# Optimization experiments

Hardware: AMD Instinct MI355X
Metric: run time of the kernel (lower is better)

The kernel has to match this reference:

```python
import jax, jax.numpy as jnp
import numpy as np

N = 16384      # number of nodes (pos rows)
S = 16384      # number of src nodes (src_pos rows)
E = 262144     # number of edges (COO entries)
D = 512        # embed_dim
H = 8          # num_heads
HD = D // H    # head_dim = 64
HID = 1024     # mlp hidden
MLP_IN = D + 3 * H  # 536
EPS = 1e-5


def layer_norm(x, g, b):
    mu = jnp.mean(x, axis=-1, keepdims=True)
    var = jnp.mean((x - mu) ** 2, axis=-1, keepdims=True)
    return (x - mu) * jax.lax.rsqrt(var + EPS) * g + b


def setup_inputs() -> dict:
    key = jax.random.key(0)
    ks = jax.random.split(key, 20)
    s = 1.0 / np.sqrt(D)
    sh = 1.0 / np.sqrt(HID)
    return {
        "x": jax.random.normal(ks[0], (N, D), jnp.float32),
        "Wq": jax.random.uniform(ks[1], (D, D), jnp.float32, -s, s),
        "bq": jnp.zeros((D,), jnp.float32),
        "Wk": jax.random.uniform(ks[2], (D, D), jnp.float32, -s, s),
        "bk": jnp.zeros((D,), jnp.float32),
        "g_att": jnp.ones((D,), jnp.float32),
        "b_att": jnp.zeros((D,), jnp.float32),
        "g_mlp": jnp.ones((D,), jnp.float32),
        "b_mlp": jnp.zeros((D,), jnp.float32),
        "W_in": jax.random.uniform(ks[3], (HID, MLP_IN), jnp.float32, -s, s),
        "b_in": jnp.zeros((HID,), jnp.float32),
        "W_out": jax.random.uniform(ks[4], (D, HID), jnp.float32, -sh, sh),
        "b_out": jnp.zeros((D,), jnp.float32),
        "att_bias": jax.random.normal(ks[5], (H, E), jnp.float32),
        "dist": jax.random.uniform(ks[6], (E,), jnp.float32, 0.5, 6.0),
        "pos": jax.random.normal(ks[7], (N, 3), jnp.float32),
        "src_pos": jax.random.normal(ks[8], (S, 3), jnp.float32),
        "row_index": jax.random.randint(ks[9], (E,), 0, N),
        "src_index": jax.random.randint(ks[10], (E,), 0, S),
        "org_to_src": jax.random.randint(ks[11], (S,), 0, N),
    }


def reference(x, Wq, bq, Wk, bk, g_att, b_att, g_mlp, b_mlp, W_in, b_in,
              W_out, b_out, att_bias, dist, pos, src_pos,
              row_index, src_index, org_to_src):
    n = x.shape[0]
    z = layer_norm(x, g_att, b_att)
    q = (z @ Wq.T + bq).reshape(n, H, HD)          # [N,H,hd]
    k = (z @ Wk.T + bk).reshape(n, H, HD)          # [N,H,hd]
    k_src = k[org_to_src]                          # [S,H,hd]
    # per-edge masked logits: q[row] . k_src[col] / sqrt(hd) + bias
    qe = q[row_index]                              # [E,H,hd]
    ke = k_src[src_index]                          # [E,H,hd]
    logits = jnp.einsum('ehd,ehd->eh', qe, ke) / jnp.sqrt(jnp.float32(HD))
    logits = logits + att_bias.T                   # [E,H]
    # segment (per-row) softmax over incident edges
    m = jax.ops.segment_max(logits, row_index, num_segments=n)
    p = jnp.exp(logits - m[row_index])
    den = jax.ops.segment_sum(p, row_index, num_segments=n)
    att = p / den[row_index]                       # [E,H]
    inv = jnp.where(dist == 0, 0.0, 1.0 / dist)[:, None]
    att = att * inv
    # sparse bmm: feat[h,row] += att * src_pos[col]; rowsum for centering
    sp = src_pos[src_index]                        # [E,3]
    feat = jax.ops.segment_sum(att[:, :, None] * sp[:, None, :],
                               row_index, num_segments=n)   # [N,H,3]
    rowsum = jax.ops.segment_sum(att, row_index, num_segments=n)  # [N,H]
    feat = feat - rowsum[:, :, None] * pos[:, None, :]
    feat = feat.reshape(n, H * 3)
    z2 = layer_norm(x, g_mlp, b_mlp)
    h = jax.nn.gelu(jnp.concatenate([z2, feat], axis=-1) @ W_in.T + b_in)
    return x + (h @ W_out.T + b_out)
```

## Files before the change

### kernel.cpp

```cpp
#include <hip/hip_runtime.h>
#include <math.h>


typedef unsigned short u16;
typedef __attribute__((ext_vector_type(8))) short bf16x8;
typedef __attribute__((ext_vector_type(4))) float f32x4;
typedef __attribute__((ext_vector_type(2))) float f32x2;

constexpr int N_NODES = 16384;
constexpr int E_EDGES = 262144;
constexpr int D = 512;
constexpr int KIN = 576;

constexpr size_t OFF_ZATT = 0;
constexpr size_t OFF_ZCAT = 16777216;
constexpr size_t OFF_WQK  = 35651584;
constexpr size_t OFF_BQK  = 36700160;
constexpr size_t OFF_WIN  = 36704256;
constexpr size_t OFF_WOUT = 37883904;
constexpr size_t OFF_QK   = 38932480;
constexpr size_t OFF_CNT  = 55709696;
constexpr size_t OFF_BKT  = 55775232;
constexpr size_t OFF_HBF  = 59969536;

static __device__ __forceinline__ u16 f2bf(float f) {
  union { float f; unsigned int u; } v; v.f = f;
  unsigned int u = v.u;
  u = u + 0x7FFFu + ((u >> 16) & 1u);
  return (u16)(u >> 16);
}
static __device__ __forceinline__ void gload16(const u16* g, u16* l) {
  __builtin_amdgcn_global_load_lds(
      (const __attribute__((address_space(1))) unsigned int*)g,
      (__attribute__((address_space(3))) unsigned int*)l, 16, 0, 0);
}

__global__ __launch_bounds__(256) void prep_weights(
    const float* __restrict__ Wq, const float* __restrict__ Wk,
    const float* __restrict__ bq, const float* __restrict__ bk,
    const float* __restrict__ W_in, const float* __restrict__ W_out,
    const int* __restrict__ row_index,
    const float* __restrict__ att_bias, const float* __restrict__ dist,
    const float* __restrict__ src_pos, const int* __restrict__ src_index,
    const int* __restrict__ org_to_src,
    u16* __restrict__ wqk, float* __restrict__ bqk,
    u16* __restrict__ win, u16* __restrict__ wout,
    int* __restrict__ cnt, int* __restrict__ bucket, float* __restrict__ rec)
{
  const int gid = blockIdx.x * 256 + threadIdx.x;
  if (gid < 512 * 1024) {
    wqk[gid]  = f2bf(gid < 512 * 512 ? Wq[gid] : Wk[gid - 512 * 512]);
    wout[gid] = f2bf(W_out[gid]);
  }
  if (gid < 1024 * KIN) {
    const int r = gid / KIN, c = gid - r * KIN;
    win[gid] = f2bf(c < 536 ? W_in[r * 536 + c] : 0.f);
  }
  if (gid < 1024) bqk[gid] = gid < 512 ? bq[gid] : bk[gid - 512];
  if (gid < E_EDGES) {
    const int r = row_index[gid];
    const int p = atomicAdd(&cnt[r], 1);
    if (p < 64) bucket[(size_t)r * 64 + p] = gid;
    const int s = src_index[gid];
    const float dv = dist[gid];
    float4 q0, q1, q2, q3;
    q0.x = att_bias[gid];
    q0.y = att_bias[(size_t)1 * E_EDGES + gid];
    q0.z = att_bias[(size_t)2 * E_EDGES + gid];
    q0.w = att_bias[(size_t)3 * E_EDGES + gid];
    q1.x = att_bias[(size_t)4 * E_EDGES + gid];
    q1.y = att_bias[(size_t)5 * E_EDGES + gid];
    q1.z = att_bias[(size_t)6 * E_EDGES + gid];
    q1.w = att_bias[(size_t)7 * E_EDGES + gid];
    q2.x = (dv == 0.f) ? 0.f : 1.f / dv;
    q2.y = src_pos[(size_t)s * 3 + 0];
    q2.z = src_pos[(size_t)s * 3 + 1];
    q2.w = src_pos[(size_t)s * 3 + 2];
    q3.x = __int_as_float(org_to_src[s]);
    q3.y = 0.f; q3.z = 0.f; q3.w = 0.f;
    float4* rg = (float4*)(rec + (size_t)gid * 16);
    rg[0] = q0; rg[1] = q1; rg[2] = q2; rg[3] = q3;
  }
}

__global__ __launch_bounds__(256) void ln_kernel(
    const float* __restrict__ x,
    const float* __restrict__ g1, const float* __restrict__ b1,
    const float* __restrict__ g2, const float* __restrict__ b2,
    u16* __restrict__ zatt, u16* __restrict__ zcat)
{
  const int row = blockIdx.x;
  const int t = threadIdx.x;
  const float2 v = *(const float2*)(x + (size_t)row * D + t * 2);
  float s = v.x + v.y;
  float s2 = v.x * v.x + v.y * v.y;
#pragma unroll
  for (int m = 1; m < 64; m <<= 1) {
    s  += __shfl_xor(s, m, 64);
    s2 += __shfl_xor(s2, m, 64);
  }
  __shared__ float red[8];
  const int wv = t >> 6;
  if ((t & 63) == 0) { red[wv] = s; red[4 + wv] = s2; }
  __syncthreads();
  s  = red[0] + red[1] + red[2] + red[3];
  s2 = red[4] + red[5] + red[6] + red[7];
  const float mu = s * (1.f / D);
  const float var = s2 * (1.f / D) - mu * mu;
  const float rs = rsqrtf(var + 1e-5f);
  const int c0 = t * 2;
  const float n0 = (v.x - mu) * rs, n1 = (v.y - mu) * rs;
  zatt[(size_t)row * D + c0]       = f2bf(n0 * g1[c0] + b1[c0]);
  zatt[(size_t)row * D + c0 + 1]   = f2bf(n1 * g1[c0 + 1] + b1[c0 + 1]);
  zcat[(size_t)row * KIN + c0]     = f2bf(n0 * g2[c0] + b2[c0]);
  zcat[(size_t)row * KIN + c0 + 1] = f2bf(n1 * g2[c0 + 1] + b2[c0 + 1]);
  if (t < 64) zcat[(size_t)row * KIN + D + t] = 0;
}

template <int EPI, int WPE>
__global__ __launch_bounds__(256, WPE) void gemm_nt(
    const u16* __restrict__ A, const u16* __restrict__ B,
    const float* __restrict__ bias, const float* __restrict__ resid,
    void* __restrict__ Cout, int M, int Nn, int K)
{
  constexpr int BM = 128, BN = 128, BK = 32;
  __shared__ __align__(16) u16 As[2 * BM * BK];
  __shared__ __align__(16) u16 Bs[2 * BN * BK];
  const int tid = threadIdx.x;
  const int lane = tid & 63;
  const int wave = tid >> 6;
  const int m0 = blockIdx.x * BM;
  const int n0 = blockIdx.y * BN;
  const int wm = (wave >> 1) * 64;
  const int wn = (wave & 1) * 64;
  const int fr = lane & 15;
  const int fq = lane >> 4;
  const int srow = lane >> 2;
  const int skoff = (lane & 3) * 8;

  f32x4 acc[4][4];
#pragma unroll
  for (int i = 0; i < 4; ++i)
#pragma unroll
    for (int j = 0; j < 4; ++j) acc[i][j] = 0.f;

  for (int k0 = 0; k0 < K; k0 += 2 * BK) {
    __syncthreads();
#pragma unroll
    for (int t = 0; t < 2; ++t) {
#pragma unroll
      for (int r = 0; r < 2; ++r) {
        const int rowbase = r * 64 + wave * 16;
        gload16(A + (size_t)(m0 + rowbase + srow) * K + k0 + t * BK + skoff,
                As + t * (BM * BK) + rowbase * BK);
        gload16(B + (size_t)(n0 + rowbase + srow) * K + k0 + t * BK + skoff,
                Bs + t * (BN * BK) + rowbase * BK);
      }
    }
    __syncthreads();
#pragma unroll
    for (int t = 0; t < 2; ++t) {
      bf16x8 af[4], bfr[4];
#pragma unroll
      for (int mi = 0; mi < 4; ++mi)
        af[mi] = *(const bf16x8*)(As + t * (BM * BK) + (wm + mi * 16 + fr) * BK + fq * 8);
#pragma unroll
      for (int ni = 0; ni < 4; ++ni)
        bfr[ni] = *(const bf16x8*)(Bs + t * (BN * BK) + (wn + ni * 16 + fr) * BK + fq * 8);
#pragma unroll
      for (int mi = 0; mi < 4; ++mi)
#pragma unroll
        for (int ni = 0; ni < 4; ++ni)
          acc[mi][ni] = __builtin_amdgcn_mfma_f32_16x16x32_bf16(af[mi], bfr[ni], acc[mi][ni], 0, 0, 0);
    }
  }

#pragma unroll
  for (int mi = 0; mi < 4; ++mi) {
#pragma unroll
    for (int ni = 0; ni < 4; ++ni) {
      const int col = n0 + wn + ni * 16 + fr;
      const float bv = bias[col];
#pragma unroll
      for (int rr = 0; rr < 4; ++rr) {
        const int row = m0 + wm + mi * 16 + fq * 4 + rr;
        float v = acc[mi][ni][rr] + bv;
        if (EPI == 1) {
          const float nu = -1.5957691216057308f * (v + 0.044715f * v * v * v);
          const float sg = __builtin_amdgcn_rcpf(1.f + __expf(nu));
          ((u16*)Cout)[(size_t)row * Nn + col] = f2bf(v * sg);
        } else if (EPI == 2) {
          ((float*)Cout)[(size_t)row * Nn + col] = v + resid[(size_t)row * Nn + col];
        } else {
          const int pk = __builtin_amdgcn_cvt_pk_fp8_f32(v, v, 0, false);
          ((unsigned char*)Cout)[(size_t)row * Nn + col] = (unsigned char)(pk & 0xFF);
        }
      }
    }
  }
}

__global__ __launch_bounds__(256) void edge_csr(
    const unsigned char* __restrict__ qk8, const float* __restrict__ rec,
    const int* __restrict__ cnt, const int* __restrict__ bucket,
    const float* __restrict__ pos, u16* __restrict__ zcat)
{
  const int lane = threadIdx.x & 63;
  const int wave = threadIdx.x >> 6;
  const int row = blockIdx.x * 4 + wave;
  const int half = lane >> 5;
  const int sub = lane & 31;
  const int h = sub >> 2, j = sub & 3;
  const int deg = min(cnt[row], 64);
  const int base = row * 64;

  const uint4 qv = *(const uint4*)(qk8 + (size_t)row * 1024 + sub * 16);
  float qf[16];
  {
    const unsigned int* qu = (const unsigned int*)&qv;
#pragma unroll
    for (int i = 0; i < 4; ++i) {
      const f32x2 lo = __builtin_amdgcn_cvt_pk_f32_fp8(qu[i], false);
      const f32x2 hi = __builtin_amdgcn_cvt_pk_f32_fp8(qu[i], true);
      qf[i * 4 + 0] = lo.x; qf[i * 4 + 1] = lo.y;
      qf[i * 4 + 2] = hi.x; qf[i * 4 + 3] = hi.y;
    }
  }

  float accA = 0.f, accB = 0.f;
  const int npair = (deg + 1) >> 1;

  bool ok0 = half < deg;
  int e0 = ok0 ? bucket[base + half] : 0;
  const float* r0 = rec + (size_t)e0 * 16;
  float bias0 = r0[h];
  float invd0 = r0[8];
  float spA0 = (j >= 2) ? r0[7 + j] : 0.f;
  float spB0 = (j == 1) ? r0[11] : 0.f;
  uint4 kv0 = *(const uint4*)(qk8 + (size_t)__float_as_int(r0[12]) * 1024 + 512 + sub * 16);

  bool ok1 = 2 + half < deg;
  int e1 = ok1 ? bucket[base + 2 + half] : 0;
  const float* r1 = rec + (size_t)e1 * 16;
  float bias1 = r1[h];
  float invd1 = r1[8];
  float spA1 = (j >= 2) ? r1[7 + j] : 0.f;
  float spB1 = (j == 1) ? r1[11] : 0.f;
  int kr1 = __float_as_int(r1[12]);

  bool ok2 = 4 + half < deg;
  int e2 = ok2 ? bucket[base + 4 + half] : 0;

  for (int i = 0; i < npair; ++i) {
    const uint4 kv1 = *(const uint4*)(qk8 + (size_t)kr1 * 1024 + 512 + sub * 16);
    const float* r2 = rec + (size_t)e2 * 16;
    const float bias2 = r2[h];
    const float invd2 = r2[8];
    const float spA2 = (j >= 2) ? r2[7 + j] : 0.f;
    const float spB2 = (j == 1) ? r2[11] : 0.f;
    const int kr2 = __float_as_int(r2[12]);
    const bool ok3 = 2 * (i + 3) + half < deg;
    const int e3 = ok3 ? bucket[base + 2 * (i + 3) + half] : 0;

    float p;
    {
      const unsigned int* ku = (const unsigned int*)&kv0;
      const f32x2 a0 = __builtin_amdgcn_cvt_pk_f32_fp8(ku[0], false);
      const f32x2 a1 = __builtin_amdgcn_cvt_pk_f32_fp8(ku[0], true);
      const f32x2 b0 = __builtin_amdgcn_cvt_pk_f32_fp8(ku[1], false);
      const f32x2 b1 = __builtin_amdgcn_cvt_pk_f32_fp8(ku[1], true);
      const f32x2 c0 = __builtin_amdgcn_cvt_pk_f32_fp8(ku[2], false);
      const f32x2 c1 = __builtin_amdgcn_cvt_pk_f32_fp8(ku[2], true);
      const f32x2 d0 = __builtin_amdgcn_cvt_pk_f32_fp8(ku[3], false);
      const f32x2 d1 = __builtin_amdgcn_cvt_pk_f32_fp8(ku[3], true);
      p = qf[0] * a0.x;
      p = fmaf(qf[1],  a0.y, p);  p = fmaf(qf[2],  a1.x, p);  p = fmaf(qf[3],  a1.y, p);
      p = fmaf(qf[4],  b0.x, p);  p = fmaf(qf[5],  b0.y, p);  p = fmaf(qf[6],  b1.x, p);
      p = fmaf(qf[7],  b1.y, p);  p = fmaf(qf[8],  c0.x, p);  p = fmaf(qf[9],  c0.y, p);
      p = fmaf(qf[10], c1.x, p);  p = fmaf(qf[11], c1.y, p);  p = fmaf(qf[12], d0.x, p);
      p = fmaf(qf[13], d0.y, p);  p = fmaf(qf[14], d1.x, p);  p = fmaf(qf[15], d1.y, p);
    }
    p += __shfl_xor(p, 1, 64);
    p += __shfl_xor(p, 2, 64);
    float pe = __expf(p * 0.125f + bias0);
    pe = ok0 ? pe : 0.f;
    const float w = pe * invd0;
    accA += (j == 0) ? pe : (j == 1) ? w : w * spA0;
    accB += w * spB0;

    ok0 = ok1; bias0 = bias1; invd0 = invd1; spA0 = spA1; spB0 = spB1; kv0 = kv1;
    ok1 = ok2; bias1 = bias2; invd1 = invd2; spA1 = spA2; spB1 = spB2; kr1 = kr2;
    ok2 = ok3; e2 = e3;
  }

  accA += __shfl_xor(accA, 32, 64);
  accB += __shfl_xor(accB, 32, 64);
  const int hb = h << 2;
  const float den  = __shfl(accA, hb + 0, 64);
  const float wsum = __shfl(accA, hb + 1, 64);
  const float wsp01 = __shfl(accA, hb + 2 + (j & 1), 64);
  const float wsp2  = __shfl(accB, hb + 1, 64);
  const float invd = (den != 0.f) ? 1.f / den : 0.f;
  const float rsum = wsum * invd;
  if (half == 0 && j < 3) {
    const float wspj = (j < 2) ? wsp01 : wsp2;
    zcat[(size_t)row * KIN + D + h * 3 + j] = f2bf(wspj * invd - rsum * pos[row * 3 + j]);
  }
}

extern "C" void kernel_launch(void* const* d_in, const int* in_sizes, int n_in,
                              void* d_out, int out_size, void* d_ws, size_t ws_size,
                              hipStream_t stream)
{
  const float* x        = (const float*)d_in[0];
  const float* Wq       = (const float*)d_in[1];
  const float* bq       = (const float*)d_in[2];
  const float* Wk       = (const float*)d_in[3];
  const float* bk       = (const float*)d_in[4];
  const float* g_att    = (const float*)d_in[5];
  const float* b_att    = (const float*)d_in[6];
  const float* g_mlp    = (const float*)d_in[7];
  const float* b_mlp    = (const float*)d_in[8];
  const float* W_in     = (const float*)d_in[9];
  const float* b_in     = (const float*)d_in[10];
  const float* W_out    = (const float*)d_in[11];
  const float* b_out    = (const float*)d_in[12];
  const float* att_bias = (const float*)d_in[13];
  const float* dist     = (const float*)d_in[14];
  const float* pos      = (const float*)d_in[15];
  const float* src_pos  = (const float*)d_in[16];
  const int* row_index  = (const int*)d_in[17];
  const int* src_index  = (const int*)d_in[18];
  const int* org_to_src = (const int*)d_in[19];

  char* ws = (char*)d_ws;
  u16*   zatt = (u16*)(ws + OFF_ZATT);
  u16*   zcat = (u16*)(ws + OFF_ZCAT);
  u16*   wqk  = (u16*)(ws + OFF_WQK);
  float* bqk  = (float*)(ws + OFF_BQK);
  u16*   win  = (u16*)(ws + OFF_WIN);
  u16*   wout = (u16*)(ws + OFF_WOUT);
  unsigned char* qk8 = (unsigned char*)(ws + OFF_QK);
  int*   cnt  = (int*)(ws + OFF_CNT);
  int*   bkt  = (int*)(ws + OFF_BKT);
  u16*   hbf  = (u16*)(ws + OFF_HBF);
  float* rec  = (float*)(ws + OFF_HBF);

  hipMemsetAsync(ws + OFF_CNT, 0, 65536, stream);

  prep_weights<<<2304, 256, 0, stream>>>(Wq, Wk, bq, bk, W_in, W_out, row_index,
                                         att_bias, dist, src_pos, src_index, org_to_src,
                                         wqk, bqk, win, wout, cnt, bkt, rec);
  ln_kernel<<<N_NODES, 256, 0, stream>>>(x, g_att, b_att, g_mlp, b_mlp, zatt, zcat);
  gemm_nt<4, 4><<<dim3(128, 8), 256, 0, stream>>>(zatt, wqk, bqk, nullptr, qk8, N_NODES, 1024, 512);
  edge_csr<<<N_NODES / 4, 256, 0, stream>>>(qk8, rec, cnt, bkt, pos, zcat);
  gemm_nt<1, 4><<<dim3(128, 8), 256, 0, stream>>>(zcat, win, b_in, nullptr, hbf, N_NODES, 1024, KIN);
  gemm_nt<2, 2><<<dim3(128, 4), 256, 0, stream>>>(hbf, wout, b_out, x, d_out, N_NODES, 512, 1024);
}
```

Before: 268.0 us.

## Add 256x256-tile 8-wave pipelined GEMM for QK and MLP-in projections

```diff
diff --git a/kernel.cpp b/kernel.cpp
--- a/kernel.cpp
+++ b/kernel.cpp
@@ -117,6 +117,144 @@
   if (t < 64) zcat[(size_t)row * KIN + D + t] = 0;
 }
 
+
+#define MM_BLK(AF, BF, NB) do {                                               \
+  __builtin_amdgcn_s_setprio(1);                                              \
+  _Pragma("unroll")                                                           \
+  for (int mi = 0; mi < 8; ++mi) {                                            \
+    acc[mi][NB]     = __builtin_amdgcn_mfma_f32_16x16x32_bf16(AF[mi], BF[0], acc[mi][NB], 0, 0, 0);     \
+    acc[mi][NB + 1] = __builtin_amdgcn_mfma_f32_16x16x32_bf16(AF[mi], BF[1], acc[mi][NB + 1], 0, 0, 0); \
+  }                                                                           \
+  __builtin_amdgcn_s_setprio(0);                                              \
+} while (0)
+
+template <int EPI>
+__global__ __launch_bounds__(512, 2) void gemm256(
+    const u16* __restrict__ A, const u16* __restrict__ B,
+    const float* __restrict__ bias,
+    void* __restrict__ Cout, int M, int Nn, int K)
+{
+  extern __shared__ __align__(16) u16 lds[];
+  const int tid = threadIdx.x;
+  const int lane = tid & 63;
+  const int wave = tid >> 6;
+  const int wave_m = wave >> 2;
+  const int wave_n = wave & 3;
+  const int m0 = blockIdx.x * 256;
+  const int n0 = blockIdx.y * 256;
+  const int fr = lane & 15;
+  const int fq = lane >> 4;
+  const int NT = K >> 6;
+
+  f32x4 acc[8][4];
+#pragma unroll
+  for (int i = 0; i < 8; ++i)
+#pragma unroll
+    for (int j = 0; j < 4; ++j) acc[i][j] = 0.f;
+
+  auto stageA = [&](int slot, int ktile, int kh) {
+    u16* base = lds + slot * 8192;
+    const int kb = ktile * 64 + kh * 32;
+#pragma unroll
+    for (int r = 0; r < 2; ++r) {
+      const int g = r * 512 + tid;
+      gload16(A + (size_t)(m0 + (g >> 2)) * K + kb + (g & 3) * 8,
+              base + (r * 512 + wave * 64) * 8);
+    }
+  };
+  auto stageB = [&](int slot, int ktile, int kh) {
+    u16* base = lds + 32768 + slot * 8192;
+    const int kb = ktile * 64 + kh * 32;
+#pragma unroll
+    for (int r = 0; r < 2; ++r) {
+      const int g = r * 512 + tid;
+      gload16(B + (size_t)(n0 + (g >> 2)) * K + kb + (g & 3) * 8,
+              base + (r * 512 + wave * 64) * 8);
+    }
+  };
+  auto ldA = [&](bf16x8 (&af)[8], int slot) {
+    const u16* p = lds + slot * 8192 + (wave_m * 128 + fr) * 32 + fq * 8;
+#pragma unroll
+    for (int mi = 0; mi < 8; ++mi)
+      af[mi] = *(const bf16x8*)(p + mi * 16 * 32);
+  };
+  auto ldB = [&](bf16x8 (&bf)[2], int slot, int nh) {
+    const u16* p = lds + 32768 + slot * 8192 + (wave_n * 64 + nh * 32 + fr) * 32 + fq * 8;
+    bf[0] = *(const bf16x8*)(p);
+    bf[1] = *(const bf16x8*)(p + 16 * 32);
+  };
+
+  stageA(0, 0, 0); stageB(0, 0, 0);
+  stageA(1, 0, 1); stageB(1, 0, 1);
+  stageA(2, 1, 0); stageB(2, 1, 0);
+  stageA(3, 1, 1);
+  asm volatile("s_waitcnt vmcnt(10)" ::: "memory");
+  __builtin_amdgcn_s_barrier();
+  asm volatile("" ::: "memory");
+
+  bf16x8 af[8], bf0[2], bf1[2];
+  for (int t = 0; t < NT; ++t) {
+    const int sa0 = (2 * t) & 3,  sa1 = (2 * t + 1) & 3;
+    const int sb1n = (2 * t + 3) & 3;
+    const int t1 = (t + 1 >= NT) ? t + 1 - NT : t + 1;
+    const int t2 = (t + 2 >= NT) ? t + 2 - NT : t + 2;
+
+    ldA(af, sa0); ldB(bf0, sa0, 0);
+    stageB(sb1n, t1, 1);
+    __builtin_amdgcn_s_barrier();
+    asm volatile("" ::: "memory");
+    MM_BLK(af, bf0, 0);
+    __builtin_amdgcn_s_barrier();
+    asm volatile("" ::: "memory");
+    ldB(bf1, sa0, 1);
+    stageA(sa0, t2, 0);
+    __builtin_amdgcn_s_barrier();
+    asm volatile("" ::: "memory");
+    MM_BLK(af, bf1, 2);
+    asm volatile("s_waitcnt vmcnt(10)" ::: "memory");
+    __builtin_amdgcn_s_barrier();
+    asm volatile("" ::: "memory");
+    ldA(af, sa1); ldB(bf0, sa1, 0);
+    stageB(sa0, t2, 0);
+    __builtin_amdgcn_s_barrier();
+    asm volatile("" ::: "memory");
+    MM_BLK(af, bf0, 0);
+    __builtin_amdgcn_s_barrier();
+    asm volatile("" ::: "memory");
+    ldB(bf1, sa1, 1);
+    stageA(sa1, t2, 1);
+    __builtin_amdgcn_s_barrier();
+    asm volatile("" ::: "memory");
+    MM_BLK(af, bf1, 2);
+    asm volatile("s_waitcnt vmcnt(10)" ::: "memory");
+    __builtin_amdgcn_s_barrier();
+    asm volatile("" ::: "memory");
+  }
+  asm volatile("s_waitcnt vmcnt(0)" ::: "memory");
+
+#pragma unroll
+  for (int mi = 0; mi < 8; ++mi) {
+#pragma unroll
+    for (int nj = 0; nj < 4; ++nj) {
+      const int col = n0 + wave_n * 64 + nj * 16 + fr;
+      const float bv = bias[col];
+#pragma unroll
+      for (int rr = 0; rr < 4; ++rr) {
+        const int row = m0 + wave_m * 128 + mi * 16 + fq * 4 + rr;
+        float v = acc[mi][nj][rr] + bv;
+        if (EPI == 1) {
+          const float nu = -1.5957691216057308f * (v + 0.044715f * v * v * v);
+          const float sg = __builtin_amdgcn_rcpf(1.f + __expf(nu));
+          ((u16*)Cout)[(size_t)row * Nn + col] = f2bf(v * sg);
+        } else {
+          const int pk = __builtin_amdgcn_cvt_pk_fp8_f32(v, v, 0, false);
+          ((unsigned char*)Cout)[(size_t)row * Nn + col] = (unsigned char)(pk & 0xFF);
+        }
+      }
+    }
+  }
+}
+
 template <int EPI, int WPE>
 __global__ __launch_bounds__(256, WPE) void gemm_nt(
     const u16* __restrict__ A, const u16* __restrict__ B,
@@ -346,14 +484,23 @@
   u16*   hbf  = (u16*)(ws + OFF_HBF);
   float* rec  = (float*)(ws + OFF_HBF);
 
+  static bool s_attr = false;
+  if (!s_attr) {
+    hipFuncSetAttribute(reinterpret_cast<const void*>(&gemm256<4>),
+                        hipFuncAttributeMaxDynamicSharedMemorySize, 131072);
+    hipFuncSetAttribute(reinterpret_cast<const void*>(&gemm256<1>),
+                        hipFuncAttributeMaxDynamicSharedMemorySize, 131072);
+    s_attr = true;
+  }
+
   hipMemsetAsync(ws + OFF_CNT, 0, 65536, stream);
 
   prep_weights<<<2304, 256, 0, stream>>>(Wq, Wk, bq, bk, W_in, W_out, row_index,
                                          att_bias, dist, src_pos, src_index, org_to_src,
                                          wqk, bqk, win, wout, cnt, bkt, rec);
   ln_kernel<<<N_NODES, 256, 0, stream>>>(x, g_att, b_att, g_mlp, b_mlp, zatt, zcat);
-  gemm_nt<4, 4><<<dim3(128, 8), 256, 0, stream>>>(zatt, wqk, bqk, nullptr, qk8, N_NODES, 1024, 512);
+  gemm256<4><<<dim3(64, 4), 512, 131072, stream>>>(zatt, wqk, bqk, qk8, N_NODES, 1024, 512);
   edge_csr<<<N_NODES / 4, 256, 0, stream>>>(qk8, rec, cnt, bkt, pos, zcat);
-  gemm_nt<1, 4><<<dim3(128, 8), 256, 0, stream>>>(zcat, win, b_in, nullptr, hbf, N_NODES, 1024, KIN);
+  gemm256<1><<<dim3(64, 4), 512, 131072, stream>>>(zcat, win, b_in, hbf, N_NODES, 1024, KIN);
   gemm_nt<2, 2><<<dim3(128, 4), 256, 0, stream>>>(hbf, wout, b_out, x, d_out, N_NODES, 512, 1024);
 }
```

Measured after the change: 263.2 us. About the same (-1.8%).
